# Kernel tuning notes

Hardware: AMD Instinct MI355X
Metric: run time of the kernel (lower is better)

The kernel has to match this reference:

```python
import jax, jax.numpy as jnp
import numpy as np

B, T = 32, 2048            # batch, longest acoustic length
SIN, HIN = 1024, 1024      # decoder-state dim, listener-output dim
KD, VD = 512, 512          # key/value projection dims
EPS = 1e-12                # F.normalize eps


def setup_inputs() -> dict:
    key = jax.random.key(0)
    ks = jax.random.split(key, 9)
    s = 0.02
    return {
        "decoder_state": jax.random.normal(ks[0], (B, SIN), dtype=jnp.float32),
        "listener_output": jax.random.normal(ks[1], (B, T, HIN), dtype=jnp.float32),
        "outputs_length": jax.random.randint(ks[2], (B,), 1, T + 1, dtype=jnp.int32),
        "Ws": jax.random.normal(ks[3], (KD, SIN), dtype=jnp.float32) * s,
        "bs": jnp.zeros((KD,), dtype=jnp.float32),
        "Wh": jax.random.normal(ks[4], (KD, HIN), dtype=jnp.float32) * s,
        "bh": jnp.zeros((KD,), dtype=jnp.float32),
        "Wv": jax.random.normal(ks[5], (VD, HIN), dtype=jnp.float32) * s,
        "bv": jnp.zeros((VD,), dtype=jnp.float32),
    }


def reference(decoder_state, listener_output, outputs_length, Ws, bs, Wh, bh, Wv, bv):
    # query: [B, KD]
    query = decoder_state @ Ws.T + bs
    # key: [B, T, KD]
    keyp = jnp.einsum('bth,kh->btk', listener_output, Wh) + bh
    # energy: [B, 1, T]
    energy = jnp.einsum('bk,btk->bt', query, keyp)[:, None, :]
    attn = jax.nn.softmax(energy, axis=2)
    # length mask; NOTE: original loop skips i==0, so sample 0 is never masked
    pos = jnp.arange(T)
    mask = (pos[None, :] < outputs_length[:, None]).astype(attn.dtype)
    mask = mask.at[0].set(1.0)
    attn = attn * mask[:, None, :]
    # L1 renormalize (F.normalize p=1, dim=2, eps=1e-12); attn >= 0
    attn = attn / jnp.maximum(jnp.sum(attn, axis=2, keepdims=True), EPS)
    # value: [B, T, VD]; context: [B, VD]
    value = jnp.einsum('bth,vh->btv', listener_output, Wv) + bv
    context = jnp.einsum('bqt,btv->bqv', attn, value)[:, 0, :]
    return context, attn
```

## Files before the change

kernel.cpp:

```cpp
#include <hip/hip_runtime.h>
#include <math.h>

#define BB 32
#define TT 2048
#define SIN 1024
#define HIN 1024
#define KD 512
#define VD 512
#define EBASE 20.0f

#define OFF_Q      0
#define OFF_W      16384
#define OFF_E      49152
#define OFF_PART   114688

__device__ __forceinline__ float dot4(float4 a, float4 b) {
  return fmaf(a.x, b.x, fmaf(a.y, b.y, fmaf(a.z, b.z, a.w * b.w)));
}

__device__ __forceinline__ float4 add4(float4 a, float4 b) {
  return make_float4(a.x + b.x, a.y + b.y, a.z + b.z, a.w + b.w);
}

__device__ __forceinline__ float wave_reduce_sum(float e) {
#pragma unroll
  for (int off = 32; off > 0; off >>= 1) e += __shfl_xor(e, off, 64);
  return e;
}

__global__ __launch_bounds__(256) void k_query(const float* __restrict__ ds,
                                               const float* __restrict__ Ws,
                                               const float* __restrict__ bs,
                                               float* __restrict__ q) {
  const int lane = threadIdx.x & 63;
  const int wid  = threadIdx.x >> 6;
  const int k    = blockIdx.x * 4 + wid;
  const float4* Wr = (const float4*)(Ws + (size_t)k * SIN);
  float4 w0 = Wr[lane], w1 = Wr[64 + lane], w2 = Wr[128 + lane], w3 = Wr[192 + lane];
  float bk = bs[k];
  for (int b = 0; b < BB; ++b) {
    const float4* dr = (const float4*)(ds + (size_t)b * SIN);
    float4 d0 = dr[lane], d1 = dr[64 + lane], d2 = dr[128 + lane], d3 = dr[192 + lane];
    float e = dot4(w0, d0) + dot4(w1, d1) + dot4(w2, d2) + dot4(w3, d3);
    e = wave_reduce_sum(e);
    if (lane == 0) q[(size_t)b * KD + k] = e + bk;
  }
}

__global__ __launch_bounds__(256) void k_w(const float* __restrict__ Wh,
                                           const float* __restrict__ q,
                                           float* __restrict__ w) {
  __shared__ float qs[8][KD];
  const int h  = blockIdx.x * 256 + threadIdx.x;
  const int b0 = blockIdx.y * 8;
#pragma unroll
  for (int r = 0; r < 16; ++r) {
    int lin = r * 256 + threadIdx.x;
    qs[lin >> 9][lin & 511] = q[(size_t)(b0 + (lin >> 9)) * KD + (lin & 511)];
  }
  __syncthreads();
  float acc[8] = {0.f, 0.f, 0.f, 0.f, 0.f, 0.f, 0.f, 0.f};
  for (int kk = 0; kk < KD; ++kk) {
    float wh = Wh[(size_t)kk * HIN + h];
#pragma unroll
    for (int i = 0; i < 8; ++i) acc[i] = fmaf(wh, qs[i][kk], acc[i]);
  }
#pragma unroll
  for (int i = 0; i < 8; ++i)
    w[(size_t)(b0 + i) * HIN + h] = acc[i];
}

__global__ __launch_bounds__(256) void k_main(const float* __restrict__ L,
                                              const float* __restrict__ wv,
                                              const int* __restrict__ lens,
                                              float* __restrict__ pen,
                                              float* __restrict__ part) {
  const int b     = blockIdx.x >> 5;
  const int chunk = blockIdx.x & 31;
  const int t0    = chunk * 64;
  const int wid   = threadIdx.x >> 6;
  const int lane  = threadIdx.x & 63;
  const int len   = lens[b];
  const bool row0 = (b == 0);

  const float4* wr = (const float4*)(wv + (size_t)b * HIN);
  float4 w0 = wr[lane], w1 = wr[64 + lane], w2 = wr[128 + lane], w3 = wr[192 + lane];

  float z = 0.f, kept = 0.f;
  float4 a0 = {0, 0, 0, 0}, a1 = {0, 0, 0, 0}, a2 = {0, 0, 0, 0}, a3 = {0, 0, 0, 0};
  const size_t rowbase = (size_t)b * TT * HIN;

  __shared__ float hdr[4][2];
  __shared__ float accs[4][1024];
  __shared__ float sp[64];

#pragma unroll 2
  for (int i = 0; i < 16; ++i) {
    const int t = t0 + i * 4 + wid;
    const float4* vr = (const float4*)(L + rowbase + (size_t)t * HIN);
    float4 v0 = vr[lane], v1 = vr[64 + lane], v2 = vr[128 + lane], v3 = vr[192 + lane];
    float e = dot4(w0, v0) + dot4(w1, v1) + dot4(w2, v2) + dot4(w3, v3);
    e = wave_reduce_sum(e);
    float p = __expf(e - EBASE);
    if (lane == 0) sp[i * 4 + wid] = p;
    float g = (row0 || t < len) ? p : 0.f;
    z += p;
    kept += g;
    a0.x = fmaf(g, v0.x, a0.x); a0.y = fmaf(g, v0.y, a0.y);
    a0.z = fmaf(g, v0.z, a0.z); a0.w = fmaf(g, v0.w, a0.w);
    a1.x = fmaf(g, v1.x, a1.x); a1.y = fmaf(g, v1.y, a1.y);
    a1.z = fmaf(g, v1.z, a1.z); a1.w = fmaf(g, v1.w, a1.w);
    a2.x = fmaf(g, v2.x, a2.x); a2.y = fmaf(g, v2.y, a2.y);
    a2.z = fmaf(g, v2.z, a2.z); a2.w = fmaf(g, v2.w, a2.w);
    a3.x = fmaf(g, v3.x, a3.x); a3.y = fmaf(g, v3.y, a3.y);
    a3.z = fmaf(g, v3.z, a3.z); a3.w = fmaf(g, v3.w, a3.w);
  }

  if (lane == 0) { hdr[wid][0] = z; hdr[wid][1] = kept; }
  float4* as = (float4*)accs[wid];
  as[lane] = a0; as[64 + lane] = a1; as[128 + lane] = a2; as[192 + lane] = a3;
  __syncthreads();
  float* pb = part + (size_t)blockIdx.x * 1028;
  if (threadIdx.x == 0) {
    pb[0] = hdr[0][0] + hdr[1][0] + hdr[2][0] + hdr[3][0];
    pb[1] = hdr[0][1] + hdr[1][1] + hdr[2][1] + hdr[3][1];
  }
  if (threadIdx.x < 64) pen[(size_t)b * TT + t0 + threadIdx.x] = sp[threadIdx.x];
#pragma unroll
  for (int i = 0; i < 4; ++i) {
    int h = threadIdx.x + 256 * i;
    pb[4 + h] = accs[0][h] + accs[1][h] + accs[2][h] + accs[3][h];
  }
}

__global__ __launch_bounds__(256) void k_fin(const float* __restrict__ part,
                                             const float* __restrict__ pen,
                                             const int* __restrict__ lens,
                                             const float* __restrict__ Wvm,
                                             const float* __restrict__ bv,
                                             float* __restrict__ out,
                                             float* __restrict__ out_attn) {
  const int b = blockIdx.x >> 2;
  const int s = blockIdx.x & 3;
  const int lane = threadIdx.x & 63;
  const int wid  = threadIdx.x >> 6;
  __shared__ float sZ[32], sK[32];
  __shared__ float sc[1024];
  if (threadIdx.x < 32) {
    const float* pb = part + (size_t)(b * 32 + threadIdx.x) * 1028;
    sZ[threadIdx.x] = pb[0]; sK[threadIdx.x] = pb[1];
  }
  __syncthreads();
  float Z = 0.f, K = 0.f;
#pragma unroll
  for (int i = 0; i < 32; ++i) { Z += sZ[i]; K += sK[i]; }
  const float kept_sum = K / Z;
  const float ks = fmaxf(kept_sum, 1e-12f);
  const float inv = 1.f / (Z * ks);
  const float rbv = kept_sum / ks;

  float4 A = {0.f, 0.f, 0.f, 0.f};
#pragma unroll
  for (int p = 0; p < 32; ++p)
    A = add4(A, *(const float4*)(part + (size_t)(b * 32 + p) * 1028 + 4 + threadIdx.x * 4));
  ((float4*)sc)[threadIdx.x] = make_float4(A.x * inv, A.y * inv, A.z * inv, A.w * inv);

  const int len = lens[b];
#pragma unroll
  for (int j = 0; j < 2; ++j) {
    int t = s * 512 + j * 256 + threadIdx.x;
    bool keep = (b == 0) || (t < len);
    float pe = pen[(size_t)b * TT + t];
    out_attn[(size_t)b * TT + t] = keep ? pe * inv : 0.f;
  }
  __syncthreads();

  const float4* scv = (const float4*)sc;
  float4 c0 = scv[lane], c1 = scv[64 + lane], c2 = scv[128 + lane], c3 = scv[192 + lane];
  for (int j = 0; j < 32; ++j) {
    const int v = s * 128 + wid * 32 + j;
    const float4* Wr = (const float4*)(Wvm + (size_t)v * HIN);
    float4 w0 = Wr[lane], w1 = Wr[64 + lane], w2 = Wr[128 + lane], w3 = Wr[192 + lane];
    float e = dot4(w0, c0) + dot4(w1, c1) + dot4(w2, c2) + dot4(w3, c3);
    e = wave_reduce_sum(e);
    if (lane == 0) out[(size_t)b * VD + v] = e + bv[v] * rbv;
  }
}

extern "C" void kernel_launch(void* const* d_in, const int* in_sizes, int n_in,
                              void* d_out, int out_size, void* d_ws, size_t ws_size,
                              hipStream_t stream) {
  const float* ds   = (const float*)d_in[0];
  const float* L    = (const float*)d_in[1];
  const int*   lens = (const int*)d_in[2];
  const float* Ws   = (const float*)d_in[3];
  const float* bs   = (const float*)d_in[4];
  const float* Wh   = (const float*)d_in[5];
  const float* Wv   = (const float*)d_in[7];
  const float* bv   = (const float*)d_in[8];
  float* out = (float*)d_out;
  float* ws  = (float*)d_ws;

  float* q    = ws + OFF_Q;
  float* w    = ws + OFF_W;
  float* pen  = ws + OFF_E;
  float* part = ws + OFF_PART;

  k_query<<<128, 256, 0, stream>>>(ds, Ws, bs, q);
  k_w    <<<dim3(4, 4), 256, 0, stream>>>(Wh, q, w);
  k_main <<<1024, 256, 0, stream>>>(L, w, lens, pen, part);
  k_fin  <<<128, 256, 0, stream>>>(part, pen, lens, Wv, bv, out, out + BB * VD);
}
```

Before: 466.7 us.

## Split final stage into reduce and Wv-stationary context projection kernels

The fused finish kernel is split in two. The first kernel reduces the per-chunk partial sums; each block now handles only its own quarter of the hidden dimension, so the partials are no longer read four times. It writes the normalized context vector and the bias scale to the workspace. A second kernel keeps each Wv row in registers and loops over all batches, so Wv is read once instead of once per batch. The cost is an extra kernel launch and a round trip of the context vector through global memory.

```diff
diff --git a/kernel.cpp b/kernel.cpp
--- a/kernel.cpp
+++ b/kernel.cpp
@@ -13,13 +13,11 @@
 #define OFF_W      16384
 #define OFF_E      49152
 #define OFF_PART   114688
+#define OFF_CTX    1167360
+#define OFF_R      1200128
 
 __device__ __forceinline__ float dot4(float4 a, float4 b) {
   return fmaf(a.x, b.x, fmaf(a.y, b.y, fmaf(a.z, b.z, a.w * b.w)));
-}
-
-__device__ __forceinline__ float4 add4(float4 a, float4 b) {
-  return make_float4(a.x + b.x, a.y + b.y, a.z + b.z, a.w + b.w);
 }
 
 __device__ __forceinline__ float wave_reduce_sum(float e) {
@@ -133,19 +131,15 @@
   }
 }
 
-__global__ __launch_bounds__(256) void k_fin(const float* __restrict__ part,
-                                             const float* __restrict__ pen,
-                                             const int* __restrict__ lens,
-                                             const float* __restrict__ Wvm,
-                                             const float* __restrict__ bv,
-                                             float* __restrict__ out,
-                                             float* __restrict__ out_attn) {
+__global__ __launch_bounds__(256) void k_reduce(const float* __restrict__ part,
+                                                const float* __restrict__ pen,
+                                                const int* __restrict__ lens,
+                                                float* __restrict__ ctx,
+                                                float* __restrict__ rb,
+                                                float* __restrict__ out_attn) {
   const int b = blockIdx.x >> 2;
   const int s = blockIdx.x & 3;
-  const int lane = threadIdx.x & 63;
-  const int wid  = threadIdx.x >> 6;
   __shared__ float sZ[32], sK[32];
-  __shared__ float sc[1024];
   if (threadIdx.x < 32) {
     const float* pb = part + (size_t)(b * 32 + threadIdx.x) * 1028;
     sZ[threadIdx.x] = pb[0]; sK[threadIdx.x] = pb[1];
@@ -157,14 +151,12 @@
   const float kept_sum = K / Z;
   const float ks = fmaxf(kept_sum, 1e-12f);
   const float inv = 1.f / (Z * ks);
-  const float rbv = kept_sum / ks;
-
-  float4 A = {0.f, 0.f, 0.f, 0.f};
+  const int h = s * 256 + threadIdx.x;
+  float A = 0.f;
 #pragma unroll
   for (int p = 0; p < 32; ++p)
-    A = add4(A, *(const float4*)(part + (size_t)(b * 32 + p) * 1028 + 4 + threadIdx.x * 4));
-  ((float4*)sc)[threadIdx.x] = make_float4(A.x * inv, A.y * inv, A.z * inv, A.w * inv);
-
+    A += part[(size_t)(b * 32 + p) * 1028 + 4 + h];
+  ctx[(size_t)b * HIN + h] = A * inv;
   const int len = lens[b];
 #pragma unroll
   for (int j = 0; j < 2; ++j) {
@@ -173,17 +165,26 @@
     float pe = pen[(size_t)b * TT + t];
     out_attn[(size_t)b * TT + t] = keep ? pe * inv : 0.f;
   }
-  __syncthreads();
-
-  const float4* scv = (const float4*)sc;
-  float4 c0 = scv[lane], c1 = scv[64 + lane], c2 = scv[128 + lane], c3 = scv[192 + lane];
-  for (int j = 0; j < 32; ++j) {
-    const int v = s * 128 + wid * 32 + j;
-    const float4* Wr = (const float4*)(Wvm + (size_t)v * HIN);
-    float4 w0 = Wr[lane], w1 = Wr[64 + lane], w2 = Wr[128 + lane], w3 = Wr[192 + lane];
+  if (s == 0 && threadIdx.x == 0) rb[b] = kept_sum / ks;
+}
+
+__global__ __launch_bounds__(256) void k_context(const float* __restrict__ Wvm,
+                                                 const float* __restrict__ bv,
+                                                 const float* __restrict__ ctx,
+                                                 const float* __restrict__ rb,
+                                                 float* __restrict__ out) {
+  const int lane = threadIdx.x & 63;
+  const int wid  = threadIdx.x >> 6;
+  const int v    = blockIdx.x * 4 + wid;
+  const float4* Wr = (const float4*)(Wvm + (size_t)v * HIN);
+  float4 w0 = Wr[lane], w1 = Wr[64 + lane], w2 = Wr[128 + lane], w3 = Wr[192 + lane];
+  const float bvv = bv[v];
+  for (int b = 0; b < BB; ++b) {
+    const float4* cr = (const float4*)(ctx + (size_t)b * HIN);
+    float4 c0 = cr[lane], c1 = cr[64 + lane], c2 = cr[128 + lane], c3 = cr[192 + lane];
     float e = dot4(w0, c0) + dot4(w1, c1) + dot4(w2, c2) + dot4(w3, c3);
     e = wave_reduce_sum(e);
-    if (lane == 0) out[(size_t)b * VD + v] = e + bv[v] * rbv;
+    if (lane == 0) out[(size_t)b * VD + v] = e + bvv * rb[b];
   }
 }
 
@@ -205,9 +206,12 @@
   float* w    = ws + OFF_W;
   float* pen  = ws + OFF_E;
   float* part = ws + OFF_PART;
-
-  k_query<<<128, 256, 0, stream>>>(ds, Ws, bs, q);
-  k_w    <<<dim3(4, 4), 256, 0, stream>>>(Wh, q, w);
-  k_main <<<1024, 256, 0, stream>>>(L, w, lens, pen, part);
-  k_fin  <<<128, 256, 0, stream>>>(part, pen, lens, Wv, bv, out, out + BB * VD);
-}
+  float* ctx  = ws + OFF_CTX;
+  float* rbuf = ws + OFF_R;
+
+  k_query  <<<128, 256, 0, stream>>>(ds, Ws, bs, q);
+  k_w      <<<dim3(4, 4), 256, 0, stream>>>(Wh, q, w);
+  k_main   <<<1024, 256, 0, stream>>>(L, w, lens, pen, part);
+  k_reduce <<<128, 256, 0, stream>>>(part, pen, lens, ctx, rbuf, out + BB * VD);
+  k_context<<<128, 256, 0, stream>>>(Wv, bv, ctx, rbuf, out);
+}
```

Result: no change. 459.3 us (-1.6%).
